# Kernel optimization log

Hardware: AMD Instinct MI355X
Metric: run time of the kernel (lower is better)

## Reference

```python
import jax, jax.numpy as jnp
import numpy as np

TOP_K = 2


def setup_inputs() -> dict:
    key = jax.random.key(0)
    k0, k1, k2, k3, k4, k5 = jax.random.split(key, 6)
    N, D_IN, D_OUT, H, G = 8192, 1024, 1024, 4096, 3
    E = 2 ** G
    x = jax.random.normal(k0, (N, D_IN), jnp.float32)
    # gate: Linear(in_dim, gate_dim, bias=False) followed by act (ReLU)
    Wg = jax.random.normal(k1, (D_IN, G), jnp.float32) * (1.0 / np.sqrt(D_IN))
    # experts: per-expert 2-layer MLP: Linear(in,hid) + ReLU + Linear(hid,out)
    W1 = jax.random.normal(k2, (E, D_IN, H), jnp.float32) * (1.0 / np.sqrt(D_IN))
    b1 = jax.random.normal(k3, (E, H), jnp.float32) * 0.01
    W2 = jax.random.normal(k4, (E, H, D_OUT), jnp.float32) * (1.0 / np.sqrt(H))
    b2 = jax.random.normal(k5, (E, D_OUT), jnp.float32) * 0.01
    return {"x": x, "Wg": Wg, "W1": W1, "b1": b1, "W2": W2, "b2": b2}


def _hypercube_mask(E, G, dtype):
    # binary(arange(2^G), G) * 2 - 1 : corners of the hypercube in {-1,+1}^G
    codes = jnp.arange(E)
    bits = (codes[:, None] >> jnp.arange(G)[None, :]) & 1  # [E, G]
    return (bits * 2 - 1).astype(dtype)


def reference(x, Wg, W1, b1, W2, b2):
    G = Wg.shape[1]
    E = W1.shape[0]
    N = x.shape[0]
    mask = _hypercube_mask(E, G, x.dtype)                 # [E, G]
    logits = jax.nn.relu(x @ Wg)                          # [N, G]
    scores = logits @ mask.T                              # [N, E] = sum_d logits*mask
    probs = jax.nn.softmax(scores, axis=1)                # softmax over experts
    topv, topi = jax.lax.top_k(probs, TOP_K)              # [N, k]
    topv = topv / topv.sum(axis=-1, keepdims=True)        # renormalize selected probs
    # dense combine weights: zero for non-selected experts (same math as gather/scatter dispatch)
    combine = jnp.zeros((N, E), x.dtype).at[jnp.arange(N)[:, None], topi].set(topv)
    out = jnp.zeros((N, W2.shape[2]), x.dtype)
    for e in range(E):  # small fixed expert count
        h = jax.nn.relu(x @ W1[e] + b1[e])                # [N, H]
        out = out + combine[:, e:e + 1] * (h @ W2[e] + b2[e])
    return out
```

## Files before the change

### kernel.cpp

```cpp
#include <hip/hip_runtime.h>

#define NTOK 8192
#define DIN  1024
#define DOUT 1024
#define HDIM 4096
#define NEXP 8
#define NPAIR (NTOK * 2)

typedef __attribute__((ext_vector_type(8))) short bf16x8;
typedef __attribute__((ext_vector_type(4))) float f32x4;

__device__ __forceinline__ unsigned short f2bf(float f) {
  union { float f; unsigned u; } v; v.f = f;
  unsigned u = v.u;
  unsigned r = (u + 0x7fffu + ((u >> 16) & 1u)) >> 16;
  return (unsigned short)r;
}

__device__ __forceinline__ void gload16(const void* g, void* l) {
  __builtin_amdgcn_global_load_lds(
      (const __attribute__((address_space(1))) unsigned int*)g,
      (__attribute__((address_space(3))) unsigned int*)l, 16, 0, 0);
}

__global__ void gate_kernel(const float* __restrict__ x, const float* __restrict__ Wg,
                            int* __restrict__ cnt, int* __restrict__ ptok,
                            float* __restrict__ pw) {
  const int lane = threadIdx.x & 63;
  const int t = blockIdx.x * 4 + (threadIdx.x >> 6);
  const float* xr = x + (size_t)t * DIN + lane * 16;
  const float* wr = Wg + (size_t)lane * 16 * 3;
  double d0 = 0, d1 = 0, d2 = 0;
#pragma unroll
  for (int j = 0; j < 16; j++) {
    double xv = xr[j];
    d0 += xv * wr[j * 3 + 0];
    d1 += xv * wr[j * 3 + 1];
    d2 += xv * wr[j * 3 + 2];
  }
#pragma unroll
  for (int o = 32; o > 0; o >>= 1) {
    d0 += __shfl_down(d0, o);
    d1 += __shfl_down(d1, o);
    d2 += __shfl_down(d2, o);
  }
  if (lane == 0) {
    double l0 = d0 > 0 ? d0 : 0, l1 = d1 > 0 ? d1 : 0, l2 = d2 > 0 ? d2 : 0;
    double s[NEXP];
#pragma unroll
    for (int e = 0; e < NEXP; e++)
      s[e] = ((e & 1) ? l0 : -l0) + ((e & 2) ? l1 : -l1) + ((e & 4) ? l2 : -l2);
    int e0 = 0;
    for (int e = 1; e < NEXP; e++) if (s[e] > s[e0]) e0 = e;
    int e1 = -1;
    for (int e = 0; e < NEXP; e++) { if (e == e0) continue; if (e1 < 0 || s[e] > s[e1]) e1 = e; }
    double w0 = 1.0 / (1.0 + exp(s[e1] - s[e0]));
    double w1 = 1.0 - w0;
    int p0 = atomicAdd(cnt + e0, 1);
    ptok[e0 * NTOK + p0] = t; pw[e0 * NTOK + p0] = (float)w0;
    int p1 = atomicAdd(cnt + e1, 1);
    ptok[e1 * NTOK + p1] = t; pw[e1 * NTOK + p1] = (float)w1;
  }
}

__global__ void scan_kernel(const int* __restrict__ cnt, int* __restrict__ off) {
  if (threadIdx.x == 0) {
    int a = 0;
    for (int e = 0; e < NEXP; e++) { off[e] = a; a += cnt[e]; }
  }
}

__global__ void cvt_bf16_kernel(const float* __restrict__ src,
                                unsigned short* __restrict__ dst, int n) {
  int i = (blockIdx.x * 256 + threadIdx.x) * 8;
  if (i >= n) return;
  float4 a = *(const float4*)(src + i);
  float4 b = *(const float4*)(src + i + 4);
  __align__(16) unsigned short t[8] = {f2bf(a.x), f2bf(a.y), f2bf(a.z), f2bf(a.w),
                                       f2bf(b.x), f2bf(b.y), f2bf(b.z), f2bf(b.w)};
  *(uint4*)(dst + i) = *(const uint4*)t;
}

__global__ void transpose_cvt(const float* __restrict__ src,
                              unsigned short* __restrict__ dst, int K, int N) {
  __shared__ float tile[64][65];
  const size_t base = (size_t)blockIdx.z * K * N;
  const float* s = src + base;
  unsigned short* d = dst + base;
  int n0 = blockIdx.x * 64, k0 = blockIdx.y * 64;
  for (int idx = threadIdx.x; idx < 64 * 16; idx += 256) {
    int r = idx >> 4, c4 = (idx & 15) * 4;
    float4 v = *(const float4*)(s + (size_t)(k0 + r) * N + n0 + c4);
    tile[r][c4 + 0] = v.x; tile[r][c4 + 1] = v.y;
    tile[r][c4 + 2] = v.z; tile[r][c4 + 3] = v.w;
  }
  __syncthreads();
  for (int idx = threadIdx.x; idx < 64 * 8; idx += 256) {
    int nl = idx >> 3, c8 = (idx & 7) * 8;
    __align__(16) unsigned short tmp[8];
#pragma unroll
    for (int j = 0; j < 8; j++) tmp[j] = f2bf(tile[c8 + j][nl]);
    *(uint4*)(d + (size_t)(n0 + nl) * K + k0 + c8) = *(const uint4*)tmp;
  }
}

__global__ __launch_bounds__(256, 4) void gemm1_kernel(
    const unsigned short* __restrict__ xbf,
    const unsigned short* __restrict__ w1t,
    const float* __restrict__ b1,
    const int* __restrict__ cnt, const int* __restrict__ off,
    const int* __restrict__ ptok,
    unsigned short* __restrict__ h)
{
  const int e = blockIdx.z;
  const int ce = cnt[e];
  if (ce == 0) return;
  const int NT = HDIM / 128;
  const int bid = blockIdx.x + NT * blockIdx.y;
  const int xcd = bid & 7;
  const int j = bid >> 3;
  const int mt = xcd + 8 * (j / NT);
  const int nt = j % NT;
  const int m0 = mt * 128;
  if (m0 >= ce) return;
  const int n0 = nt * 128;
  const int oe = off[e];
  __shared__ __align__(16) unsigned short lA[2][128 * 32];
  __shared__ __align__(16) unsigned short lB[2][128 * 32];
  const int tid = threadIdx.x;
  const int lane = tid & 63;
  const int wv = tid >> 6;
  const int wr = wv >> 1, wc = wv & 1;

  const int c0 = tid, c1 = tid + 256;
  const int ra0 = c0 >> 2, ra1 = c1 >> 2;
  const int ka0 = (c0 & 3) * 8, ka1 = (c1 & 3) * 8;
  const int ta0 = ptok[e * NTOK + min(m0 + ra0, ce - 1)];
  const int ta1 = ptok[e * NTOK + min(m0 + ra1, ce - 1)];
  const unsigned short* ga0 = xbf + (size_t)ta0 * DIN + ka0;
  const unsigned short* ga1 = xbf + (size_t)ta1 * DIN + ka1;
  const unsigned short* wb = w1t + (size_t)e * HDIM * DIN;
  const unsigned short* gb0 = wb + (size_t)(n0 + ra0) * DIN + ka0;
  const unsigned short* gb1 = wb + (size_t)(n0 + ra1) * DIN + ka1;

  f32x4 acc[4][4] = {};
  const int fr = lane & 15;
  const int fk = (lane >> 4) * 8;

#define STAGE1(buf, kk)                                   \
  do {                                                    \
    gload16(ga0 + (kk), &lA[buf][c0 * 8]);                \
    gload16(ga1 + (kk), &lA[buf][c1 * 8]);                \
    gload16(gb0 + (kk), &lB[buf][c0 * 8]);                \
    gload16(gb1 + (kk), &lB[buf][c1 * 8]);                \
  } while (0)

#define COMPUTE1(buf)                                                        \
  do {                                                                       \
    bf16x8 a[4], b[4];                                                       \
    _Pragma("unroll") for (int i = 0; i < 4; i++)                            \
      a[i] = *(const bf16x8*)(&lA[buf][(wr * 64 + i * 16 + fr) * 32 + fk]);  \
    _Pragma("unroll") for (int i = 0; i < 4; i++)                            \
      b[i] = *(const bf16x8*)(&lB[buf][(wc * 64 + i * 16 + fr) * 32 + fk]);  \
    _Pragma("unroll") for (int mi = 0; mi < 4; mi++)                         \
      _Pragma("unroll") for (int ni = 0; ni < 4; ni++)                       \
        acc[mi][ni] = __builtin_amdgcn_mfma_f32_16x16x32_bf16(               \
            a[mi], b[ni], acc[mi][ni], 0, 0, 0);                             \
  } while (0)

  STAGE1(0, 0);
  asm volatile("s_waitcnt vmcnt(0)" ::: "memory");
  __syncthreads();
  int cur = 0;
  for (int k0 = 32; k0 < DIN; k0 += 32) {
    STAGE1(cur ^ 1, k0);
    COMPUTE1(cur);
    asm volatile("s_waitcnt vmcnt(0)" ::: "memory");
    __syncthreads();
    cur ^= 1;
  }
  COMPUTE1(cur);

  const int cr = (lane >> 4) * 4;
  const int cc = lane & 15;
#pragma unroll
  for (int mi = 0; mi < 4; mi++) {
    int rbase = wr * 64 + mi * 16 + cr;
#pragma unroll
    for (int r = 0; r < 4; r++) {
      int grow = m0 + rbase + r;
      if (grow >= ce) continue;
      size_t hoff = (size_t)(oe + grow) * HDIM;
#pragma unroll
      for (int ni = 0; ni < 4; ni++) {
        int col = n0 + wc * 64 + ni * 16 + cc;
        float v = acc[mi][ni][r] + b1[e * HDIM + col];
        h[hoff + col] = f2bf(v > 0.f ? v : 0.f);
      }
    }
  }
}

__global__ __launch_bounds__(256, 4) void gemm2_kernel(
    const unsigned short* __restrict__ h,
    const unsigned short* __restrict__ w2t,
    const float* __restrict__ b2,
    const int* __restrict__ cnt, const int* __restrict__ off,
    const int* __restrict__ ptok, const float* __restrict__ pw,
    float* __restrict__ out)
{
  const int e = blockIdx.z;
  const int ce = cnt[e];
  if (ce == 0) return;
  const int NT = DOUT / 128;
  const int bid = blockIdx.x + NT * blockIdx.y;
  const int xcd = bid & 7;
  const int j = bid >> 3;
  const int mt = xcd + 8 * (j / NT);
  const int nt = j % NT;
  const int m0 = mt * 128;
  if (m0 >= ce) return;
  const int n0 = nt * 128;
  const int oe = off[e];
  __shared__ __align__(16) unsigned short lA[2][128 * 32];
  __shared__ __align__(16) unsigned short lB[2][128 * 32];
  const int tid = threadIdx.x;
  const int lane = tid & 63;
  const int wv = tid >> 6;
  const int wr = wv >> 1, wc = wv & 1;

  const int c0 = tid, c1 = tid + 256;
  const int ra0 = c0 >> 2, ra1 = c1 >> 2;
  const int ka0 = (c0 & 3) * 8, ka1 = (c1 & 3) * 8;
  const int rc0 = min(m0 + ra0, ce - 1), rc1 = min(m0 + ra1, ce - 1);
  const unsigned short* ga0 = h + (size_t)(oe + rc0) * HDIM + ka0;
  const unsigned short* ga1 = h + (size_t)(oe + rc1) * HDIM + ka1;
  const unsigned short* wb = w2t + (size_t)e * DOUT * HDIM;
  const unsigned short* gb0 = wb + (size_t)(n0 + ra0) * HDIM + ka0;
  const unsigned short* gb1 = wb + (size_t)(n0 + ra1) * HDIM + ka1;

  f32x4 acc[4][4] = {};
  const int fr = lane & 15;
  const int fk = (lane >> 4) * 8;

#define STAGE2(buf, kk)                                   \
  do {                                                    \
    gload16(ga0 + (kk), &lA[buf][c0 * 8]);                \
    gload16(ga1 + (kk), &lA[buf][c1 * 8]);                \
    gload16(gb0 + (kk), &lB[buf][c0 * 8]);                \
    gload16(gb1 + (kk), &lB[buf][c1 * 8]);                \
  } while (0)

  STAGE2(0, 0);
  asm volatile("s_waitcnt vmcnt(0)" ::: "memory");
  __syncthreads();
  int cur = 0;
  for (int k0 = 32; k0 < HDIM; k0 += 32) {
    STAGE2(cur ^ 1, k0);
    {
      bf16x8 a[4], b[4];
#pragma unroll
      for (int i = 0; i < 4; i++)
        a[i] = *(const bf16x8*)(&lA[cur][(wr * 64 + i * 16 + fr) * 32 + fk]);
#pragma unroll
      for (int i = 0; i < 4; i++)
        b[i] = *(const bf16x8*)(&lB[cur][(wc * 64 + i * 16 + fr) * 32 + fk]);
#pragma unroll
      for (int mi = 0; mi < 4; mi++)
#pragma unroll
        for (int ni = 0; ni < 4; ni++)
          acc[mi][ni] = __builtin_amdgcn_mfma_f32_16x16x32_bf16(a[mi], b[ni], acc[mi][ni], 0, 0, 0);
    }
    asm volatile("s_waitcnt vmcnt(0)" ::: "memory");
    __syncthreads();
    cur ^= 1;
  }
  {
    bf16x8 a[4], b[4];
#pragma unroll
    for (int i = 0; i < 4; i++)
      a[i] = *(const bf16x8*)(&lA[cur][(wr * 64 + i * 16 + fr) * 32 + fk]);
#pragma unroll
    for (int i = 0; i < 4; i++)
      b[i] = *(const bf16x8*)(&lB[cur][(wc * 64 + i * 16 + fr) * 32 + fk]);
#pragma unroll
    for (int mi = 0; mi < 4; mi++)
#pragma unroll
      for (int ni = 0; ni < 4; ni++)
        acc[mi][ni] = __builtin_amdgcn_mfma_f32_16x16x32_bf16(a[mi], b[ni], acc[mi][ni], 0, 0, 0);
  }

  const int cr = (lane >> 4) * 4;
  const int cc = lane & 15;
#pragma unroll
  for (int mi = 0; mi < 4; mi++) {
    int rbase = wr * 64 + mi * 16 + cr;
#pragma unroll
    for (int r = 0; r < 4; r++) {
      int grow = m0 + rbase + r;
      if (grow >= ce) continue;
      int idx = e * NTOK + grow;
      int token = ptok[idx];
      float w = pw[idx];
#pragma unroll
      for (int ni = 0; ni < 4; ni++) {
        int col = n0 + wc * 64 + ni * 16 + cc;
        float v = (acc[mi][ni][r] + b2[e * DOUT + col]) * w;
        atomicAdd(out + (size_t)token * DOUT + col, v);
      }
    }
  }
}

extern "C" void kernel_launch(void* const* d_in, const int* in_sizes, int n_in,
                              void* d_out, int out_size, void* d_ws, size_t ws_size,
                              hipStream_t stream) {
  const float* x  = (const float*)d_in[0];
  const float* Wg = (const float*)d_in[1];
  const float* W1 = (const float*)d_in[2];
  const float* b1 = (const float*)d_in[3];
  const float* W2 = (const float*)d_in[4];
  const float* b2 = (const float*)d_in[5];
  float* out = (float*)d_out;

  char* ws = (char*)d_ws;
  size_t o = 0;
  auto nxt = [&](size_t b) { char* p = ws + o; o = (o + b + 255) & ~(size_t)255; return p; };
  int* cnt = (int*)nxt(64);
  int* off = (int*)nxt(64);
  int* ptok = (int*)nxt((size_t)NEXP * NTOK * 4);
  float* pw = (float*)nxt((size_t)NEXP * NTOK * 4);
  unsigned short* xbf = (unsigned short*)nxt((size_t)NTOK * DIN * 2);
  unsigned short* w1t = (unsigned short*)nxt((size_t)NEXP * HDIM * DIN * 2);
  unsigned short* w2t = (unsigned short*)nxt((size_t)NEXP * DOUT * HDIM * 2);
  unsigned short* hbuf = (unsigned short*)nxt((size_t)NPAIR * HDIM * 2);

  hipMemsetAsync(cnt, 0, 64, stream);
  hipMemsetAsync(out, 0, (size_t)NTOK * DOUT * 4, stream);

  gate_kernel<<<NTOK / 4, 256, 0, stream>>>(x, Wg, cnt, ptok, pw);
  scan_kernel<<<1, 64, 0, stream>>>(cnt, off);
  cvt_bf16_kernel<<<(NTOK * DIN / 8) / 256, 256, 0, stream>>>(x, xbf, NTOK * DIN);
  transpose_cvt<<<dim3(HDIM / 64, DIN / 64, NEXP), 256, 0, stream>>>(W1, w1t, DIN, HDIM);
  transpose_cvt<<<dim3(DOUT / 64, HDIM / 64, NEXP), 256, 0, stream>>>(W2, w2t, HDIM, DOUT);

  gemm1_kernel<<<dim3(HDIM / 128, NTOK / 128, NEXP), 256, 0, stream>>>(
      xbf, w1t, b1, cnt, off, ptok, hbuf);
  gemm2_kernel<<<dim3(DOUT / 128, NTOK / 128, NEXP), 256, 0, stream>>>(
      hbuf, w2t, b2, cnt, off, ptok, pw, out);
}
```

Measured before the change: 834.4 us.

## Enlarge expert GEMM tiles to 256x256 with 1024-thread blocks and expert-interleaved grid

```diff
diff --git a/kernel.cpp b/kernel.cpp
--- a/kernel.cpp
+++ b/kernel.cpp
@@ -104,7 +104,7 @@
   }
 }
 
-__global__ __launch_bounds__(256, 4) void gemm1_kernel(
+__global__ __launch_bounds__(1024, 2) void gemm1_kernel(
     const unsigned short* __restrict__ xbf,
     const unsigned short* __restrict__ w1t,
     const float* __restrict__ b1,
@@ -112,47 +112,38 @@
     const int* __restrict__ ptok,
     unsigned short* __restrict__ h)
 {
-  const int e = blockIdx.z;
+  const int bid = blockIdx.x;
+  const int e = bid & 7;
   const int ce = cnt[e];
-  if (ce == 0) return;
-  const int NT = HDIM / 128;
-  const int bid = blockIdx.x + NT * blockIdx.y;
-  const int xcd = bid & 7;
-  const int j = bid >> 3;
-  const int mt = xcd + 8 * (j / NT);
-  const int nt = j % NT;
-  const int m0 = mt * 128;
+  const int idx = bid >> 3;
+  const int mt = idx >> 4;
+  const int nt = idx & 15;
+  const int m0 = mt * 256;
   if (m0 >= ce) return;
-  const int n0 = nt * 128;
+  const int n0 = nt * 256;
   const int oe = off[e];
-  __shared__ __align__(16) unsigned short lA[2][128 * 32];
-  __shared__ __align__(16) unsigned short lB[2][128 * 32];
+  __shared__ __align__(16) unsigned short lA[2][256 * 32];
+  __shared__ __align__(16) unsigned short lB[2][256 * 32];
   const int tid = threadIdx.x;
   const int lane = tid & 63;
   const int wv = tid >> 6;
-  const int wr = wv >> 1, wc = wv & 1;
-
-  const int c0 = tid, c1 = tid + 256;
-  const int ra0 = c0 >> 2, ra1 = c1 >> 2;
-  const int ka0 = (c0 & 3) * 8, ka1 = (c1 & 3) * 8;
-  const int ta0 = ptok[e * NTOK + min(m0 + ra0, ce - 1)];
-  const int ta1 = ptok[e * NTOK + min(m0 + ra1, ce - 1)];
-  const unsigned short* ga0 = xbf + (size_t)ta0 * DIN + ka0;
-  const unsigned short* ga1 = xbf + (size_t)ta1 * DIN + ka1;
+  const int wr = wv >> 2, wc = wv & 3;
+
+  const int ra = tid >> 2;
+  const int ka = (tid & 3) * 8;
+  const int ta = ptok[e * NTOK + min(m0 + ra, ce - 1)];
+  const unsigned short* ga = xbf + (size_t)ta * DIN + ka;
   const unsigned short* wb = w1t + (size_t)e * HDIM * DIN;
-  const unsigned short* gb0 = wb + (size_t)(n0 + ra0) * DIN + ka0;
-  const unsigned short* gb1 = wb + (size_t)(n0 + ra1) * DIN + ka1;
+  const unsigned short* gb = wb + (size_t)(n0 + ra) * DIN + ka;
 
   f32x4 acc[4][4] = {};
   const int fr = lane & 15;
   const int fk = (lane >> 4) * 8;
 
-#define STAGE1(buf, kk)                                   \
-  do {                                                    \
-    gload16(ga0 + (kk), &lA[buf][c0 * 8]);                \
-    gload16(ga1 + (kk), &lA[buf][c1 * 8]);                \
-    gload16(gb0 + (kk), &lB[buf][c0 * 8]);                \
-    gload16(gb1 + (kk), &lB[buf][c1 * 8]);                \
+#define STAGE1(buf, kk)                          \
+  do {                                           \
+    gload16(ga + (kk), &lA[buf][tid * 8]);       \
+    gload16(gb + (kk), &lB[buf][tid * 8]);       \
   } while (0)
 
 #define COMPUTE1(buf)                                                        \
@@ -201,7 +192,7 @@
   }
 }
 
-__global__ __launch_bounds__(256, 4) void gemm2_kernel(
+__global__ __launch_bounds__(1024, 2) void gemm2_kernel(
     const unsigned short* __restrict__ h,
     const unsigned short* __restrict__ w2t,
     const float* __restrict__ b2,
@@ -209,46 +200,51 @@
     const int* __restrict__ ptok, const float* __restrict__ pw,
     float* __restrict__ out)
 {
-  const int e = blockIdx.z;
+  const int bid = blockIdx.x;
+  const int e = bid & 7;
   const int ce = cnt[e];
-  if (ce == 0) return;
-  const int NT = DOUT / 128;
-  const int bid = blockIdx.x + NT * blockIdx.y;
-  const int xcd = bid & 7;
-  const int j = bid >> 3;
-  const int mt = xcd + 8 * (j / NT);
-  const int nt = j % NT;
-  const int m0 = mt * 128;
+  const int idx = bid >> 3;
+  const int mt = idx >> 2;
+  const int nt = idx & 3;
+  const int m0 = mt * 256;
   if (m0 >= ce) return;
-  const int n0 = nt * 128;
+  const int n0 = nt * 256;
   const int oe = off[e];
-  __shared__ __align__(16) unsigned short lA[2][128 * 32];
-  __shared__ __align__(16) unsigned short lB[2][128 * 32];
+  __shared__ __align__(16) unsigned short lA[2][256 * 32];
+  __shared__ __align__(16) unsigned short lB[2][256 * 32];
   const int tid = threadIdx.x;
   const int lane = tid & 63;
   const int wv = tid >> 6;
-  const int wr = wv >> 1, wc = wv & 1;
-
-  const int c0 = tid, c1 = tid + 256;
-  const int ra0 = c0 >> 2, ra1 = c1 >> 2;
-  const int ka0 = (c0 & 3) * 8, ka1 = (c1 & 3) * 8;
-  const int rc0 = min(m0 + ra0, ce - 1), rc1 = min(m0 + ra1, ce - 1);
-  const unsigned short* ga0 = h + (size_t)(oe + rc0) * HDIM + ka0;
-  const unsigned short* ga1 = h + (size_t)(oe + rc1) * HDIM + ka1;
-  const unsigned short* wb = w2t + (size_t)e * DOUT * HDIM;
-  const unsigned short* gb0 = wb + (size_t)(n0 + ra0) * HDIM + ka0;
-  const unsigned short* gb1 = wb + (size_t)(n0 + ra1) * HDIM + ka1;
+  const int wr = wv >> 2, wc = wv & 3;
+
+  const int ra = tid >> 2;
+  const int ka = (tid & 3) * 8;
+  const int rc = min(m0 + ra, ce - 1);
+  const unsigned short* ga = h + (size_t)(oe + rc) * HDIM + ka;
+  const unsigned short* wbp = w2t + (size_t)e * DOUT * HDIM;
+  const unsigned short* gb = wbp + (size_t)(n0 + ra) * HDIM + ka;
 
   f32x4 acc[4][4] = {};
   const int fr = lane & 15;
   const int fk = (lane >> 4) * 8;
 
-#define STAGE2(buf, kk)                                   \
-  do {                                                    \
-    gload16(ga0 + (kk), &lA[buf][c0 * 8]);                \
-    gload16(ga1 + (kk), &lA[buf][c1 * 8]);                \
-    gload16(gb0 + (kk), &lB[buf][c0 * 8]);                \
-    gload16(gb1 + (kk), &lB[buf][c1 * 8]);                \
+#define STAGE2(buf, kk)                          \
+  do {                                           \
+    gload16(ga + (kk), &lA[buf][tid * 8]);       \
+    gload16(gb + (kk), &lB[buf][tid * 8]);       \
+  } while (0)
+
+#define COMPUTE2(buf)                                                        \
+  do {                                                                       \
+    bf16x8 a[4], b[4];                                                       \
+    _Pragma("unroll") for (int i = 0; i < 4; i++)                            \
+      a[i] = *(const bf16x8*)(&lA[buf][(wr * 64 + i * 16 + fr) * 32 + fk]);  \
+    _Pragma("unroll") for (int i = 0; i < 4; i++)                            \
+      b[i] = *(const bf16x8*)(&lB[buf][(wc * 64 + i * 16 + fr) * 32 + fk]);  \
+    _Pragma("unroll") for (int mi = 0; mi < 4; mi++)                         \
+      _Pragma("unroll") for (int ni = 0; ni < 4; ni++)                       \
+        acc[mi][ni] = __builtin_amdgcn_mfma_f32_16x16x32_bf16(               \
+            a[mi], b[ni], acc[mi][ni], 0, 0, 0);                             \
   } while (0)
 
   STAGE2(0, 0);
@@ -257,38 +253,12 @@
   int cur = 0;
   for (int k0 = 32; k0 < HDIM; k0 += 32) {
     STAGE2(cur ^ 1, k0);
-    {
-      bf16x8 a[4], b[4];
-#pragma unroll
-      for (int i = 0; i < 4; i++)
-        a[i] = *(const bf16x8*)(&lA[cur][(wr * 64 + i * 16 + fr) * 32 + fk]);
-#pragma unroll
-      for (int i = 0; i < 4; i++)
-        b[i] = *(const bf16x8*)(&lB[cur][(wc * 64 + i * 16 + fr) * 32 + fk]);
-#pragma unroll
-      for (int mi = 0; mi < 4; mi++)
-#pragma unroll
-        for (int ni = 0; ni < 4; ni++)
-          acc[mi][ni] = __builtin_amdgcn_mfma_f32_16x16x32_bf16(a[mi], b[ni], acc[mi][ni], 0, 0, 0);
-    }
+    COMPUTE2(cur);
     asm volatile("s_waitcnt vmcnt(0)" ::: "memory");
     __syncthreads();
     cur ^= 1;
   }
-  {
-    bf16x8 a[4], b[4];
-#pragma unroll
-    for (int i = 0; i < 4; i++)
-      a[i] = *(const bf16x8*)(&lA[cur][(wr * 64 + i * 16 + fr) * 32 + fk]);
-#pragma unroll
-    for (int i = 0; i < 4; i++)
-      b[i] = *(const bf16x8*)(&lB[cur][(wc * 64 + i * 16 + fr) * 32 + fk]);
-#pragma unroll
-    for (int mi = 0; mi < 4; mi++)
-#pragma unroll
-      for (int ni = 0; ni < 4; ni++)
-        acc[mi][ni] = __builtin_amdgcn_mfma_f32_16x16x32_bf16(a[mi], b[ni], acc[mi][ni], 0, 0, 0);
-  }
+  COMPUTE2(cur);
 
   const int cr = (lane >> 4) * 4;
   const int cc = lane & 15;
@@ -299,9 +269,9 @@
     for (int r = 0; r < 4; r++) {
       int grow = m0 + rbase + r;
       if (grow >= ce) continue;
-      int idx = e * NTOK + grow;
-      int token = ptok[idx];
-      float w = pw[idx];
+      int pidx = e * NTOK + grow;
+      int token = ptok[pidx];
+      float w = pw[pidx];
 #pragma unroll
       for (int ni = 0; ni < 4; ni++) {
         int col = n0 + wc * 64 + ni * 16 + cc;
@@ -344,8 +314,8 @@
   transpose_cvt<<<dim3(HDIM / 64, DIN / 64, NEXP), 256, 0, stream>>>(W1, w1t, DIN, HDIM);
   transpose_cvt<<<dim3(DOUT / 64, HDIM / 64, NEXP), 256, 0, stream>>>(W2, w2t, HDIM, DOUT);
 
-  gemm1_kernel<<<dim3(HDIM / 128, NTOK / 128, NEXP), 256, 0, stream>>>(
+  gemm1_kernel<<<8 * (NTOK / 256) * (HDIM / 256), 1024, 0, stream>>>(
       xbf, w1t, b1, cnt, off, ptok, hbuf);
-  gemm2_kernel<<<dim3(DOUT / 128, NTOK / 128, NEXP), 256, 0, stream>>>(
+  gemm2_kernel<<<8 * (NTOK / 256) * (DOUT / 256), 1024, 0, stream>>>(
       hbuf, w2t, b2, cnt, off, ptok, pw, out);
 }
```

Measured after the change: 984.3 us. +18.0%, slower.
